# Optimization experiments

Hardware: AMD Instinct MI355X
Metric: run time of the kernel (lower is better)

The kernel has to match this reference:

```python
import jax, jax.numpy as jnp
import numpy as np

V, T, C, H, L = 32000, 1024, 768, 12, 6
HS = C // H
B = 4
EPS = 1e-5


def layernorm(x, g, b):
    mu = jnp.mean(x, axis=-1, keepdims=True)
    var = jnp.mean(jnp.square(x - mu), axis=-1, keepdims=True)
    return (x - mu) * jax.lax.rsqrt(var + EPS) * g + b


def setup_inputs() -> dict:
    key = jax.random.key(0)
    ks = iter(jax.random.split(key, 24))
    s = lambda *sh: jax.random.normal(next(ks), sh, dtype=jnp.float32) * 0.02
    inp = {
        "tokens": jax.random.randint(next(ks), (B, T), 0, V, dtype=jnp.int64),
        "tok_emb": s(V, C),
        "pos_emb": s(T, C),
        "ln1_g": jnp.ones((L, C), jnp.float32), "ln1_b": jnp.zeros((L, C), jnp.float32),
        "wq": s(L, C, C), "wk": s(L, C, C), "wv": s(L, C, C),
        "wo": s(L, C, C), "bo": jnp.zeros((L, C), jnp.float32),
        "ln2_g": jnp.ones((L, C), jnp.float32), "ln2_b": jnp.zeros((L, C), jnp.float32),
        "w1": s(L, C, 4 * C), "b1": jnp.zeros((L, 4 * C), jnp.float32),
        "w2": s(L, 4 * C, C), "b2": jnp.zeros((L, C), jnp.float32),
        "lnf_g": jnp.ones((C,), jnp.float32), "lnf_b": jnp.zeros((C,), jnp.float32),
        "lm_w": s(C, V), "lm_b": jnp.zeros((V,), jnp.float32),
    }
    return inp


def reference(tokens, tok_emb, pos_emb, ln1_g, ln1_b, wq, wk, wv, wo, bo,
              ln2_g, ln2_b, w1, b1, w2, b2, lnf_g, lnf_b, lm_w, lm_b):
    x = tok_emb[tokens] + pos_emb[:T]  # [B,T,C]
    causal = jnp.tril(jnp.ones((T, T), bool))
    scale = HS ** -0.5
    for l in range(L):
        h = layernorm(x, ln1_g[l], ln1_b[l])
        q = (h @ wq[l]).reshape(B, T, H, HS)
        k = (h @ wk[l]).reshape(B, T, H, HS)
        v = (h @ wv[l]).reshape(B, T, H, HS)
        att = jnp.einsum("bthd,bshd->bhts", q, k) * scale
        att = jnp.where(causal, att, -jnp.inf)
        wei = jax.nn.softmax(att, axis=-1)
        o = jnp.einsum("bhts,bshd->bthd", wei, v).reshape(B, T, C)
        x = o @ wo[l] + bo[l] + x
        h2 = layernorm(x, ln2_g[l], ln2_b[l])
        x = jax.nn.relu(h2 @ w1[l] + b1[l]) @ w2[l] + b2[l] + x
    x = layernorm(x, lnf_g, lnf_b)
    logits = x @ lm_w + lm_b  # [B,T,V]
    return logits
```

## Files before the change

### kernel.cpp

```cpp
#include <hip/hip_runtime.h>

static constexpr int kV = 32000, kT = 1024, kC = 768, kH = 12, kL = 6, kB = 4;
static constexpr int kF = 3072;
static constexpr int kM = kB * kT;
static constexpr float kNEG = -30000.f;

typedef __attribute__((ext_vector_type(8))) __bf16 bf16x8;
typedef __attribute__((ext_vector_type(4))) float  f32x4;

#define DEV __device__ __forceinline__

DEV void gload16(const void* g, void* l) {
  __builtin_amdgcn_global_load_lds((__attribute__((address_space(1))) void*)(g),
                                   (__attribute__((address_space(3))) void*)(l), 16, 0, 0);
}

__global__ __launch_bounds__(192) void embed_k(const int* __restrict__ tokens,
                                               const float* __restrict__ tok_emb,
                                               const float* __restrict__ pos_emb,
                                               float* __restrict__ x) {
  int row = blockIdx.x, tid = threadIdx.x;
  int tok = tokens[row];
  int t   = row & (kT - 1);
  const float4* te = (const float4*)(tok_emb + (size_t)tok * kC);
  const float4* pe = (const float4*)(pos_emb + (size_t)t * kC);
  float4 a = te[tid], p = pe[tid];
  float4 r; r.x = a.x + p.x; r.y = a.y + p.y; r.z = a.z + p.z; r.w = a.w + p.w;
  ((float4*)(x + (size_t)row * kC))[tid] = r;
}

__global__ __launch_bounds__(192) void ln_k(const float* __restrict__ x,
                                            const float* __restrict__ g,
                                            const float* __restrict__ b,
                                            __bf16* __restrict__ out) {
  int row = blockIdx.x, tid = threadIdx.x;
  float4 v = ((const float4*)(x + (size_t)row * kC))[tid];
  float s = v.x + v.y + v.z + v.w;
#pragma unroll
  for (int m = 1; m < 64; m <<= 1) s += __shfl_xor(s, m, 64);
  __shared__ float red1[3], red2[3];
  int wid = tid >> 6;
  if ((tid & 63) == 0) red1[wid] = s;
  __syncthreads();
  float mu = (red1[0] + red1[1] + red1[2]) * (1.f / kC);
  float d0 = v.x - mu, d1 = v.y - mu, d2 = v.z - mu, d3 = v.w - mu;
  float q = d0 * d0 + d1 * d1 + d2 * d2 + d3 * d3;
#pragma unroll
  for (int m = 1; m < 64; m <<= 1) q += __shfl_xor(q, m, 64);
  if ((tid & 63) == 0) red2[wid] = q;
  __syncthreads();
  float var = (red2[0] + red2[1] + red2[2]) * (1.f / kC);
  float rs = rsqrtf(var + 1e-5f);
  float4 gv = ((const float4*)g)[tid];
  float4 bv = ((const float4*)b)[tid];
  float o0 = d0 * rs * gv.x + bv.x;
  float o1 = d1 * rs * gv.y + bv.y;
  float o2 = d2 * rs * gv.z + bv.z;
  float o3 = d3 * rs * gv.w + bv.w;
  ushort4 pk;
  unsigned short* pp = (unsigned short*)&pk;
  __bf16 t0 = (__bf16)o0; pp[0] = *(unsigned short*)&t0;
  __bf16 t1 = (__bf16)o1; pp[1] = *(unsigned short*)&t1;
  __bf16 t2 = (__bf16)o2; pp[2] = *(unsigned short*)&t2;
  __bf16 t3 = (__bf16)o3; pp[3] = *(unsigned short*)&t3;
  ((ushort4*)(out + (size_t)row * kC))[tid] = pk;
}

__global__ __launch_bounds__(256) void convT_k(const float* __restrict__ in,
                                               __bf16* __restrict__ out,
                                               int R, int Cc, size_t in_ls, size_t out_ls) {
  __shared__ float tile[32][33];
  const float* inp  = in  + (size_t)blockIdx.z * in_ls;
  __bf16*      outp = out + (size_t)blockIdx.z * out_ls;
  int r0 = blockIdx.y * 32, c0 = blockIdx.x * 32;
  int tx = threadIdx.x & 31, ty = threadIdx.x >> 5;
#pragma unroll
  for (int i = 0; i < 32; i += 8)
    tile[ty + i][tx] = inp[(size_t)(r0 + ty + i) * Cc + c0 + tx];
  __syncthreads();
  int wx = threadIdx.x & 15, wy = threadIdx.x >> 4;
#pragma unroll
  for (int i = 0; i < 32; i += 16) {
    int oc = wy + i;
    __bf16 a = (__bf16)tile[wx * 2][oc];
    __bf16 c = (__bf16)tile[wx * 2 + 1][oc];
    ushort2 pk;
    unsigned short* pp = (unsigned short*)&pk;
    pp[0] = *(unsigned short*)&a;
    pp[1] = *(unsigned short*)&c;
    *(ushort2*)(&outp[(size_t)(c0 + oc) * R + r0 + wx * 2]) = pk;
  }
}

__global__ __launch_bounds__(256) void convT3_k(const float* __restrict__ wq,
                                                const float* __restrict__ wk,
                                                const float* __restrict__ wv,
                                                __bf16* __restrict__ qkvT) {
  __shared__ float tile[32][33];
  int z = blockIdx.z, layer = z / 3, which = z % 3;
  const float* inp = (which == 0 ? wq : which == 1 ? wk : wv) + (size_t)layer * kC * kC;
  __bf16* outp = qkvT + (size_t)layer * 3 * kC * kC + (size_t)which * kC * kC;
  int r0 = blockIdx.y * 32, c0 = blockIdx.x * 32;
  int tx = threadIdx.x & 31, ty = threadIdx.x >> 5;
#pragma unroll
  for (int i = 0; i < 32; i += 8)
    tile[ty + i][tx] = inp[(size_t)(r0 + ty + i) * kC + c0 + tx];
  __syncthreads();
  int wx = threadIdx.x & 15, wy = threadIdx.x >> 4;
#pragma unroll
  for (int i = 0; i < 32; i += 16) {
    int oc = wy + i;
    __bf16 a = (__bf16)tile[wx * 2][oc];
    __bf16 c = (__bf16)tile[wx * 2 + 1][oc];
    ushort2 pk;
    unsigned short* pp = (unsigned short*)&pk;
    pp[0] = *(unsigned short*)&a;
    pp[1] = *(unsigned short*)&c;
    *(ushort2*)(&outp[(size_t)(c0 + oc) * kC + r0 + wx * 2]) = pk;
  }
}

DEV void tile_decode(int gx, int gy, int& mt, int& nt) {
  int nwg  = gx * gy;
  int wgid = blockIdx.y * gx + blockIdx.x;
  int q8 = nwg >> 3;
  int xcd = wgid & 7, loc = wgid >> 3;
  int sid = xcd * q8 + loc;
  int band = gx << 3;
  int c = sid / band, rem = sid % band;
  nt = rem >> 3;
  mt = (c << 3) + (rem & 7);
}

__global__ __launch_bounds__(512, 1) void gemmHD_k(const __bf16* __restrict__ A,
                                                   const __bf16* __restrict__ Bt,
                                                   const float* __restrict__ bias,
                                                   float* __restrict__ Cout,
                                                   int M, int N, int K) {
  __shared__ char lds[131072];
  int tid = threadIdx.x, lane = tid & 63, wid = tid >> 6;
  int wm = wid >> 2, wn = wid & 3;
  int mt, ntile;
  tile_decode(gridDim.x, gridDim.y, mt, ntile);
  int m0 = mt * 256, n0 = ntile * 256;
  int fr = lane & 15, fg = lane >> 4;
  f32x4 acc[8][4] = {};
  const size_t ldab = (size_t)K * 2;
  int nt = K >> 6;

  auto STAGE = [&](char* base, int t) {
    int k0 = t << 6;
#pragma unroll
    for (int it = 0; it < 4; ++it) {
      int oo  = tid * 16 + it * 8192;
      int row = oo >> 7;
      int cb  = (oo & 127) ^ ((row & 7) << 4);
      gload16((const char*)A + (size_t)(m0 + row) * ldab + (size_t)k0 * 2 + cb,
              base + it * 8192 + wid * 1024);
    }
#pragma unroll
    for (int it = 0; it < 4; ++it) {
      int oo  = tid * 16 + it * 8192;
      int row = oo >> 7;
      int cb  = (oo & 127) ^ ((row & 7) << 4);
      gload16((const char*)Bt + (size_t)(n0 + row) * ldab + (size_t)k0 * 2 + cb,
              base + 32768 + it * 8192 + wid * 1024);
    }
  };

  STAGE(lds, 0);
  asm volatile("s_waitcnt vmcnt(0)" ::: "memory");
  __builtin_amdgcn_sched_barrier(0);
  __builtin_amdgcn_s_barrier();

  for (int t = 0; t < nt; ++t) {
    char* base = lds + (t & 1) * 65536;
    const char* Ab = base;
    const char* Bb = base + 32768;
    if (t + 1 < nt) STAGE(lds + ((t + 1) & 1) * 65536, t + 1);

    __builtin_amdgcn_s_setprio(1);
    bf16x8 bfr[4];
#pragma unroll
    for (int p = 0; p < 4; ++p) {
      const int ks = p >> 1, mh = p & 1;
      const int cc = ks * 64 + fg * 16;
      if (mh == 0) {
#pragma unroll
        for (int n = 0; n < 4; ++n) {
          int row = wn * 64 + n * 16 + fr;
          bfr[n] = *(const bf16x8*)(Bb + row * 128 + (cc ^ ((row & 7) << 4)));
        }
      }
      bf16x8 af[4];
#pragma unroll
      for (int i = 0; i < 4; ++i) {
        int row = wm * 128 + mh * 64 + i * 16 + fr;
        af[i] = *(const bf16x8*)(Ab + row * 128 + (cc ^ ((row & 7) << 4)));
      }
#pragma unroll
      for (int i = 0; i < 4; ++i)
#pragma unroll
        for (int n = 0; n < 4; ++n)
          acc[mh * 4 + i][n] = __builtin_amdgcn_mfma_f32_16x16x32_bf16(
              af[i], bfr[n], acc[mh * 4 + i][n], 0, 0, 0);
    }
    __builtin_amdgcn_s_setprio(0);

    __builtin_amdgcn_s_barrier();
    if (t + 1 < nt)
      asm volatile("s_waitcnt vmcnt(0)" ::: "memory");
    __builtin_amdgcn_sched_barrier(0);
    __builtin_amdgcn_s_barrier();
  }

#pragma unroll
  for (int mi = 0; mi < 8; ++mi) {
#pragma unroll
    for (int n = 0; n < 4; ++n) {
      int cg  = n0 + wn * 64 + n * 16 + fr;
      int rgb = m0 + wm * 128 + mi * 16 + fg * 4;
      float bv = bias[cg];
#pragma unroll
      for (int r = 0; r < 4; ++r)
        Cout[(size_t)(rgb + r) * N + cg] = acc[mi][n][r] + bv;
    }
  }
}

template <int EPI>
__global__ __launch_bounds__(256) void gemm128_k(const __bf16* __restrict__ A,
                                                 const __bf16* __restrict__ Bt,
                                                 const float* __restrict__ bias,
                                                 const float* res,
                                                 void* Cout,
                                                 int M, int N, int K) {
  __shared__ char lds[65536];
  int tid = threadIdx.x, lane = tid & 63, wid = tid >> 6;
  int wr = wid >> 1, wc = wid & 1;
  int mt, ntile;
  tile_decode(gridDim.x, gridDim.y, mt, ntile);
  int m0 = mt * 128, n0 = ntile * 128;
  int fr = lane & 15, fg = lane >> 4;
  f32x4 acc[4][4] = {};
  const size_t ldab = (size_t)K * 2;

  auto STAGE = [&](int buf, int t) {
    int k0 = t << 6;
    char* base = lds + buf * 32768;
#pragma unroll
    for (int it = 0; it < 4; ++it) {
      int oo  = tid * 16 + it * 4096;
      int row = oo >> 7;
      int cb  = (oo & 127) ^ ((row & 7) << 4);
      gload16((const char*)A  + (size_t)(m0 + row) * ldab + (size_t)k0 * 2 + cb,
              base + it * 4096 + wid * 1024);
      gload16((const char*)Bt + (size_t)(n0 + row) * ldab + (size_t)k0 * 2 + cb,
              base + 16384 + it * 4096 + wid * 1024);
    }
  };
  auto COMPUTE = [&](int buf) {
    char* base = lds + buf * 32768;
#pragma unroll
    for (int kk = 0; kk < 2; ++kk) {
      int cb = (kk * 64 + (fg << 4)) ^ ((lane & 7) << 4);
      bf16x8 af[4], bfr[4];
#pragma unroll
      for (int i = 0; i < 4; ++i) {
        af[i]  = *(const bf16x8*)(base         + (wr * 64 + i * 16 + fr) * 128 + cb);
        bfr[i] = *(const bf16x8*)(base + 16384 + (wc * 64 + i * 16 + fr) * 128 + cb);
      }
#pragma unroll
      for (int i = 0; i < 4; ++i)
#pragma unroll
        for (int j = 0; j < 4; ++j)
          acc[i][j] = __builtin_amdgcn_mfma_f32_16x16x32_bf16(af[i], bfr[j], acc[i][j], 0, 0, 0);
    }
  };

  int nt = K >> 6;
  STAGE(0, 0);
  STAGE(1, 1);
  asm volatile("s_waitcnt vmcnt(8)" ::: "memory");
  __builtin_amdgcn_sched_barrier(0);
  __builtin_amdgcn_s_barrier();
  int cur = 0;
  for (int t = 0; t < nt; ++t) {
    __builtin_amdgcn_s_setprio(1);
    COMPUTE(cur);
    __builtin_amdgcn_s_setprio(0);
    if (t + 1 < nt) {
      __builtin_amdgcn_s_barrier();
      if (t + 2 < nt) {
        STAGE(cur, t + 2);
        asm volatile("s_waitcnt vmcnt(8)" ::: "memory");
      } else {
        asm volatile("s_waitcnt vmcnt(0)" ::: "memory");
      }
      __builtin_amdgcn_sched_barrier(0);
      __builtin_amdgcn_s_barrier();
      cur ^= 1;
    }
  }

#pragma unroll
  for (int i = 0; i < 4; ++i) {
#pragma unroll
    for (int j = 0; j < 4; ++j) {
      int cg  = n0 + wc * 64 + j * 16 + fr;
      int rgb = m0 + wr * 64 + i * 16 + fg * 4;
      if constexpr (EPI == 4) {
        if (n0 < 1536) {
#pragma unroll
          for (int r = 0; r < 4; ++r)
            ((__bf16*)Cout)[(size_t)(rgb + r) * 1536 + cg] = (__bf16)acc[i][j][r];
        } else {
          int d = cg - 1536;
          ushort4 pk;
          unsigned short* pp = (unsigned short*)&pk;
#pragma unroll
          for (int r = 0; r < 4; ++r) {
            __bf16 bv = (__bf16)acc[i][j][r];
            pp[r] = *(unsigned short*)&bv;
          }
          __bf16* vT = (__bf16*)const_cast<float*>(res);
          *(ushort4*)(vT + (size_t)d * kM + rgb) = pk;
        }
      } else {
        float bv = bias[cg];
#pragma unroll
        for (int r = 0; r < 4; ++r) {
          float v = acc[i][j][r] + bv;
          ((__bf16*)Cout)[(size_t)(rgb + r) * N + cg] = (__bf16)fmaxf(v, 0.f);
        }
      }
    }
  }
}

__global__ __launch_bounds__(256) void gemm64_k(const __bf16* __restrict__ A,
                                                const __bf16* __restrict__ Bt,
                                                const float* __restrict__ bias,
                                                const float* res,
                                                float* __restrict__ Cout,
                                                int M, int N, int K) {
  __shared__ char lds[49152];
  int tid = threadIdx.x, lane = tid & 63, wid = tid >> 6;
  int wr = wid >> 1, wc = wid & 1;
  int mt, ntile;
  tile_decode(gridDim.x, gridDim.y, mt, ntile);
  int m0 = mt * 128, n0 = ntile * 64;
  int fr = lane & 15, fg = lane >> 4;
  f32x4 acc[4][2] = {};
  const size_t ldab = (size_t)K * 2;

  auto STAGE = [&](int buf, int t) {
    int k0 = t << 6;
    char* base = lds + buf * 24576;
#pragma unroll
    for (int it = 0; it < 4; ++it) {
      int oo  = tid * 16 + it * 4096;
      int row = oo >> 7;
      int cb  = (oo & 127) ^ ((row & 7) << 4);
      gload16((const char*)A + (size_t)(m0 + row) * ldab + (size_t)k0 * 2 + cb,
              base + it * 4096 + wid * 1024);
    }
#pragma unroll
    for (int it = 0; it < 2; ++it) {
      int oo  = tid * 16 + it * 4096;
      int row = oo >> 7;
      int cb  = (oo & 127) ^ ((row & 7) << 4);
      gload16((const char*)Bt + (size_t)(n0 + row) * ldab + (size_t)k0 * 2 + cb,
              base + 16384 + it * 4096 + wid * 1024);
    }
  };
  auto COMPUTE = [&](int buf) {
    char* base = lds + buf * 24576;
#pragma unroll
    for (int kk = 0; kk < 2; ++kk) {
      int cb = (kk * 64 + (fg << 4)) ^ ((lane & 7) << 4);
      bf16x8 af[4], bfr[2];
#pragma unroll
      for (int i = 0; i < 4; ++i)
        af[i] = *(const bf16x8*)(base + (wr * 64 + i * 16 + fr) * 128 + cb);
#pragma unroll
      for (int j = 0; j < 2; ++j)
        bfr[j] = *(const bf16x8*)(base + 16384 + (wc * 32 + j * 16 + fr) * 128 + cb);
#pragma unroll
      for (int i = 0; i < 4; ++i)
#pragma unroll
        for (int j = 0; j < 2; ++j)
          acc[i][j] = __builtin_amdgcn_mfma_f32_16x16x32_bf16(af[i], bfr[j], acc[i][j], 0, 0, 0);
    }
  };

  int nt = K >> 6;
  STAGE(0, 0);
  STAGE(1, 1);
  asm volatile("s_waitcnt vmcnt(6)" ::: "memory");
  __builtin_amdgcn_sched_barrier(0);
  __builtin_amdgcn_s_barrier();
  int cur = 0;
  for (int t = 0; t < nt; ++t) {
    __builtin_amdgcn_s_setprio(1);
    COMPUTE(cur);
    __builtin_amdgcn_s_setprio(0);
    if (t + 1 < nt) {
      __builtin_amdgcn_s_barrier();
      if (t + 2 < nt) {
        STAGE(cur, t + 2);
        asm volatile("s_waitcnt vmcnt(6)" ::: "memory");
      } else {
        asm volatile("s_waitcnt vmcnt(0)" ::: "memory");
      }
      __builtin_amdgcn_sched_barrier(0);
      __builtin_amdgcn_s_barrier();
      cur ^= 1;
    }
  }

#pragma unroll
  for (int i = 0; i < 4; ++i) {
#pragma unroll
    for (int j = 0; j < 2; ++j) {
      int cg  = n0 + wc * 32 + j * 16 + fr;
      int rgb = m0 + wr * 64 + i * 16 + fg * 4;
      float bv = bias[cg];
#pragma unroll
      for (int r = 0; r < 4; ++r) {
        float v = acc[i][j][r] + bv;
        size_t idx = (size_t)(rgb + r) * N + cg;
        Cout[idx] = v + res[idx];
      }
    }
  }
}

__global__ __launch_bounds__(256) void attn_k(const __bf16* __restrict__ qk,
                                              const __bf16* __restrict__ vT,
                                              __bf16* __restrict__ optr) {
  __shared__ char lds[40960];
  int tid = threadIdx.x, lane = tid & 63, wid = tid >> 6;
  int hh = blockIdx.y, bb = blockIdx.z;
  int band = (bb * 12 + hh) >> 4;
  int xx = blockIdx.x;
  int qt;
  if (band == 0)      qt = ((xx & 7) << 1) | (xx >> 3);
  else if (band == 1) qt = (xx < 8) ? (7 - xx) : (23 - xx);
  else                qt = 15 - xx;
  size_t rowbase = (size_t)bb * kT;
  int qr = qt * 64 + wid * 16;
  char* Psw = lds + 32768 + wid * 2048;

  bf16x8 qf[2];
  {
    const __bf16* p = qk + (rowbase + qr + (lane & 15)) * (2 * kC) + hh * 64 + ((lane >> 4) * 8);
    qf[0] = *(const bf16x8*)p;
    qf[1] = *(const bf16x8*)(p + 32);
  }
  f32x4 oacc[4] = {};
  float mrun[4] = {kNEG, kNEG, kNEG, kNEG};
  float lrun[4] = {0.f, 0.f, 0.f, 0.f};

  bf16x8 kr[2], vr[2];
  auto LOADT = [&](int st) {
    int s0 = st * 64;
#pragma unroll
    for (int it = 0; it < 2; ++it) {
      int oo  = tid * 16 + it * 4096;
      int row = oo >> 7;
      int cb  = (oo & 127) ^ ((row & 7) << 4);
      kr[it] = *(const bf16x8*)((const char*)qk +
                 ((rowbase + s0 + row) * (2 * kC) + kC + hh * 64) * 2 + cb);
      vr[it] = *(const bf16x8*)((const char*)vT +
                 ((size_t)(hh * 64 + row) * kM + rowbase + s0) * 2 + cb);
    }
  };
  auto WRITET = [&](int buf) {
    char* b = lds + buf * 16384;
#pragma unroll
    for (int it = 0; it < 2; ++it) {
      int oo = tid * 16 + it * 4096;
      *(bf16x8*)(b + oo)        = kr[it];
      *(bf16x8*)(b + 8192 + oo) = vr[it];
    }
  };

  LOADT(0);
  WRITET(0);
  if (qt >= 1) LOADT(1);

  for (int st = 0; st <= qt; ++st) {
    int cur = st & 1;
    char* kb = lds + cur * 16384;
    char* vb = kb + 8192;
    __syncthreads();
    if (st + 1 <= qt) {
      WRITET(cur ^ 1);
      if (st + 2 <= qt) LOADT(st + 2);
    }

    int s0 = st * 64;
    f32x4 sacc[4] = {};
#pragma unroll
    for (int kk = 0; kk < 2; ++kk) {
      int cb = (kk * 64 + ((lane >> 4) << 4)) ^ ((lane & 7) << 4);
#pragma unroll
      for (int j = 0; j < 4; ++j) {
        bf16x8 kf = *(const bf16x8*)(kb + (j * 16 + (lane & 15)) * 128 + cb);
        sacc[j] = __builtin_amdgcn_mfma_f32_16x16x32_bf16(qf[kk], kf, sacc[j], 0, 0, 0);
      }
    }

    float pv[4][4], vm[4] = {kNEG, kNEG, kNEG, kNEG};
#pragma unroll
    for (int j = 0; j < 4; ++j) {
      int scol = s0 + j * 16 + (lane & 15);
#pragma unroll
      for (int r = 0; r < 4; ++r) {
        int qrow = qr + (lane >> 4) * 4 + r;
        float sv = sacc[j][r] * 0.125f;
        if (scol > qrow) sv = kNEG;
        pv[j][r] = sv;
        vm[r] = fmaxf(vm[r], sv);
      }
    }
#pragma unroll
    for (int r = 0; r < 4; ++r) {
      float v = vm[r];
      v = fmaxf(v, __shfl_xor(v, 1, 64)); v = fmaxf(v, __shfl_xor(v, 2, 64));
      v = fmaxf(v, __shfl_xor(v, 4, 64)); v = fmaxf(v, __shfl_xor(v, 8, 64));
      float mnew = fmaxf(mrun[r], v);
      float sc = __expf(mrun[r] - mnew);
      mrun[r] = mnew;
      lrun[r] *= sc;
      oacc[0][r] *= sc; oacc[1][r] *= sc; oacc[2][r] *= sc; oacc[3][r] *= sc;
      float rsum = 0.f;
#pragma unroll
      for (int j = 0; j < 4; ++j) {
        float p = __expf(pv[j][r] - mnew);
        pv[j][r] = p;
        rsum += p;
      }
      rsum += __shfl_xor(rsum, 1, 64); rsum += __shfl_xor(rsum, 2, 64);
      rsum += __shfl_xor(rsum, 4, 64); rsum += __shfl_xor(rsum, 8, 64);
      lrun[r] += rsum;
    }

#pragma unroll
    for (int j = 0; j < 4; ++j)
#pragma unroll
      for (int r = 0; r < 4; ++r) {
        int rloc = (lane >> 4) * 4 + r;
        int cbyt = (2 * (j * 16 + (lane & 15))) ^ ((rloc & 7) << 4);
        *(__bf16*)(Psw + rloc * 128 + cbyt) = (__bf16)pv[j][r];
      }

#pragma unroll
    for (int kk = 0; kk < 2; ++kk) {
      int cb = (kk * 64 + ((lane >> 4) << 4)) ^ ((lane & 7) << 4);
      bf16x8 pf = *(const bf16x8*)(Psw + (lane & 15) * 128 + cb);
#pragma unroll
      for (int j = 0; j < 4; ++j) {
        bf16x8 vf = *(const bf16x8*)(vb + (j * 16 + (lane & 15)) * 128 + cb);
        oacc[j] = __builtin_amdgcn_mfma_f32_16x16x32_bf16(pf, vf, oacc[j], 0, 0, 0);
      }
    }
  }

#pragma unroll
  for (int r = 0; r < 4; ++r) {
    float inv = lrun[r] > 0.f ? 1.f / lrun[r] : 0.f;
#pragma unroll
    for (int j = 0; j < 4; ++j) {
      int cg = hh * 64 + j * 16 + (lane & 15);
      int rg = qr + (lane >> 4) * 4 + r;
      optr[(rowbase + rg) * kC + cg] = (__bf16)(oacc[j][r] * inv);
    }
  }
}

extern "C" void kernel_launch(void* const* d_in, const int* in_sizes, int n_in,
                              void* d_out, int out_size, void* d_ws, size_t ws_size,
                              hipStream_t stream) {
  (void)in_sizes; (void)n_in; (void)out_size; (void)ws_size;
  const int*   tokens  = (const int*)  d_in[0];
  const float* tok_emb = (const float*)d_in[1];
  const float* pos_emb = (const float*)d_in[2];
  const float* ln1_g   = (const float*)d_in[3];
  const float* ln1_b   = (const float*)d_in[4];
  const float* wq      = (const float*)d_in[5];
  const float* wk      = (const float*)d_in[6];
  const float* wv      = (const float*)d_in[7];
  const float* wo      = (const float*)d_in[8];
  const float* bo      = (const float*)d_in[9];
  const float* ln2_g   = (const float*)d_in[10];
  const float* ln2_b   = (const float*)d_in[11];
  const float* w1      = (const float*)d_in[12];
  const float* b1      = (const float*)d_in[13];
  const float* w2      = (const float*)d_in[14];
  const float* b2      = (const float*)d_in[15];
  const float* lnf_g   = (const float*)d_in[16];
  const float* lnf_b   = (const float*)d_in[17];
  const float* lm_w    = (const float*)d_in[18];
  const float* lm_b    = (const float*)d_in[19];
  float* out = (float*)d_out;

  char* ws = (char*)d_ws;
  size_t off = 0;
  auto alloc = [&](size_t bytes) -> char* {
    char* p = ws + off; off += (bytes + 255) & ~(size_t)255; return p;
  };
  float*  x    = (float*) alloc((size_t)kM * kC * 4);
  __bf16* h    = (__bf16*)alloc((size_t)kM * kC * 2);
  __bf16* qkvT = (__bf16*)alloc((size_t)kL * 3 * kC * kC * 2);
  __bf16* woT  = (__bf16*)alloc((size_t)kL * kC * kC * 2);
  __bf16* w1T  = (__bf16*)alloc((size_t)kL * kC * kF * 2);
  __bf16* w2T  = (__bf16*)alloc((size_t)kL * kC * kF * 2);
  __bf16* qkb  = (__bf16*)alloc((size_t)kM * 2 * kC * 2);
  __bf16* vTb  = (__bf16*)alloc((size_t)kC * kM * 2);
  __bf16* ob   = (__bf16*)alloc((size_t)kM * kC * 2);
  __bf16* ffb  = (__bf16*)alloc((size_t)kM * kF * 2);
  __bf16* lmwT = qkb;

  dim3 blk(256), blk512(512);
  convT3_k<<<dim3(kC/32, kC/32, 3*kL), blk, 0, stream>>>(wq, wk, wv, qkvT);
  convT_k<<<dim3(kC/32, kC/32, kL), blk, 0, stream>>>(wo, woT, kC, kC, (size_t)kC*kC, (size_t)kC*kC);
  convT_k<<<dim3(kF/32, kC/32, kL), blk, 0, stream>>>(w1, w1T, kC, kF, (size_t)kC*kF, (size_t)kC*kF);
  convT_k<<<dim3(kC/32, kF/32, kL), blk, 0, stream>>>(w2, w2T, kF, kC, (size_t)kC*kF, (size_t)kC*kF);

  embed_k<<<kM, 192, 0, stream>>>(tokens, tok_emb, pos_emb, x);

  for (int l = 0; l < kL; ++l) {
    ln_k<<<kM, 192, 0, stream>>>(x, ln1_g + l*kC, ln1_b + l*kC, h);
    gemm128_k<4><<<dim3(3*kC/128, kM/128), blk, 0, stream>>>(
        h, qkvT + (size_t)l*3*kC*kC, nullptr, (const float*)vTb, qkb, kM, 3*kC, kC);
    attn_k<<<dim3(kT/64, kH, kB), blk, 0, stream>>>(qkb, vTb, ob);
    gemm64_k<<<dim3(kC/64, kM/128), blk, 0, stream>>>(ob, woT + (size_t)l*kC*kC, bo + l*kC, x, x, kM, kC, kC);
    ln_k<<<kM, 192, 0, stream>>>(x, ln2_g + l*kC, ln2_b + l*kC, h);
    gemm128_k<1><<<dim3(kF/128, kM/128), blk, 0, stream>>>(h, w1T + (size_t)l*kC*kF, b1 + l*kF, nullptr, ffb, kM, kF, kC);
    gemm64_k<<<dim3(kC/64, kM/128), blk, 0, stream>>>(ffb, w2T + (size_t)l*kC*kF, b2 + l*kC, x, x, kM, kC, kF);
  }
  convT_k<<<dim3(kV/32, kC/32, 1), blk, 0, stream>>>(lm_w, lmwT, kC, kV, 0, 0);
  ln_k<<<kM, 192, 0, stream>>>(x, lnf_g, lnf_b, h);
  gemmHD_k<<<dim3(kV/256, kM/256), blk512, 0, stream>>>(h, lmwT, lm_b, out, kM, kV, kC);
}
```

Baseline: 1.229 ms.

## Restructure 256x256 GEMM main loop into quadrant-staged ping-pong pipeline

```diff
diff --git a/kernel.cpp b/kernel.cpp
--- a/kernel.cpp
+++ b/kernel.cpp
@@ -148,71 +148,105 @@
   const size_t ldab = (size_t)K * 2;
   int nt = K >> 6;
 
-  auto STAGE = [&](char* base, int t) {
+  auto STAGEH = [&](int buf, int gr, const __bf16* src, int srow0, int t) {
     int k0 = t << 6;
-#pragma unroll
-    for (int it = 0; it < 4; ++it) {
+    char* base = lds + buf * 65536 + gr * 16384;
+#pragma unroll
+    for (int it = 0; it < 2; ++it) {
       int oo  = tid * 16 + it * 8192;
       int row = oo >> 7;
       int cb  = (oo & 127) ^ ((row & 7) << 4);
-      gload16((const char*)A + (size_t)(m0 + row) * ldab + (size_t)k0 * 2 + cb,
+      gload16((const char*)src + (size_t)(srow0 + row) * ldab + (size_t)k0 * 2 + cb,
               base + it * 8192 + wid * 1024);
     }
-#pragma unroll
-    for (int it = 0; it < 4; ++it) {
-      int oo  = tid * 16 + it * 8192;
-      int row = oo >> 7;
-      int cb  = (oo & 127) ^ ((row & 7) << 4);
-      gload16((const char*)Bt + (size_t)(n0 + row) * ldab + (size_t)k0 * 2 + cb,
-              base + 32768 + it * 8192 + wid * 1024);
-    }
-  };
-
-  STAGE(lds, 0);
-  asm volatile("s_waitcnt vmcnt(0)" ::: "memory");
+  };
+
+  bf16x8 aA[4][2], bB[2][2];
+  auto LDA = [&](int buf, int mh) {
+    const char* Ab = lds + buf * 65536 + wm * 16384;
+#pragma unroll
+    for (int mi = 0; mi < 4; ++mi)
+#pragma unroll
+      for (int k = 0; k < 2; ++k) {
+        int lr = mh * 64 + mi * 16 + fr;
+        aA[mi][k] = *(const bf16x8*)(Ab + lr * 128 + ((k * 64 + fg * 16) ^ ((lr & 7) << 4)));
+      }
+  };
+  auto LDB = [&](int buf, int nh) {
+    const char* Bb = lds + buf * 65536 + 32768 + (wn >> 1) * 16384;
+    int blr = (wn & 1) * 64;
+#pragma unroll
+    for (int nj = 0; nj < 2; ++nj)
+#pragma unroll
+      for (int k = 0; k < 2; ++k) {
+        int lr = blr + nh * 32 + nj * 16 + fr;
+        bB[nj][k] = *(const bf16x8*)(Bb + lr * 128 + ((k * 64 + fg * 16) ^ ((lr & 7) << 4)));
+      }
+  };
+  auto MFMAQ = [&](int mh, int nh) {
+    __builtin_amdgcn_s_setprio(1);
+#pragma unroll
+    for (int mi = 0; mi < 4; ++mi)
+#pragma unroll
+      for (int nj = 0; nj < 2; ++nj)
+#pragma unroll
+        for (int k = 0; k < 2; ++k)
+          acc[mh * 4 + mi][nh * 2 + nj] = __builtin_amdgcn_mfma_f32_16x16x32_bf16(
+              aA[mi][k], bB[nj][k], acc[mh * 4 + mi][nh * 2 + nj], 0, 0, 0);
+    __builtin_amdgcn_s_setprio(0);
+  };
+
+#define BAR() do { __builtin_amdgcn_s_barrier(); __builtin_amdgcn_sched_barrier(0); } while (0)
+
+  STAGEH(0, 0, A,  m0,       0);
+  STAGEH(0, 1, A,  m0 + 128, 0);
+  STAGEH(0, 2, Bt, n0,       0);
+  STAGEH(0, 3, Bt, n0 + 128, 0);
+  if (nt > 1) {
+    STAGEH(1, 0, A,  m0,       1);
+    STAGEH(1, 1, A,  m0 + 128, 1);
+    asm volatile("s_waitcnt vmcnt(4)" ::: "memory");
+  } else {
+    asm volatile("s_waitcnt vmcnt(0)" ::: "memory");
+  }
   __builtin_amdgcn_sched_barrier(0);
   __builtin_amdgcn_s_barrier();
 
   for (int t = 0; t < nt; ++t) {
-    char* base = lds + (t & 1) * 65536;
-    const char* Ab = base;
-    const char* Bb = base + 32768;
-    if (t + 1 < nt) STAGE(lds + ((t + 1) & 1) * 65536, t + 1);
-
-    __builtin_amdgcn_s_setprio(1);
-    bf16x8 bfr[4];
-#pragma unroll
-    for (int p = 0; p < 4; ++p) {
-      const int ks = p >> 1, mh = p & 1;
-      const int cc = ks * 64 + fg * 16;
-      if (mh == 0) {
-#pragma unroll
-        for (int n = 0; n < 4; ++n) {
-          int row = wn * 64 + n * 16 + fr;
-          bfr[n] = *(const bf16x8*)(Bb + row * 128 + (cc ^ ((row & 7) << 4)));
-        }
-      }
-      bf16x8 af[4];
-#pragma unroll
-      for (int i = 0; i < 4; ++i) {
-        int row = wm * 128 + mh * 64 + i * 16 + fr;
-        af[i] = *(const bf16x8*)(Ab + row * 128 + (cc ^ ((row & 7) << 4)));
-      }
-#pragma unroll
-      for (int i = 0; i < 4; ++i)
-#pragma unroll
-        for (int n = 0; n < 4; ++n)
-          acc[mh * 4 + i][n] = __builtin_amdgcn_mfma_f32_16x16x32_bf16(
-              af[i], bfr[n], acc[mh * 4 + i][n], 0, 0, 0);
-    }
-    __builtin_amdgcn_s_setprio(0);
-
+    int buf = t & 1;
+    LDA(buf, 0); LDB(buf, 0);
+    if (t + 1 < nt) {
+      STAGEH(buf ^ 1, 2, Bt, n0,       t + 1);
+      STAGEH(buf ^ 1, 3, Bt, n0 + 128, t + 1);
+    }
+    BAR();
+    MFMAQ(0, 0);
+    BAR();
+    LDB(buf, 1);
+    BAR();
+    MFMAQ(0, 1);
+    BAR();
+    LDA(buf, 1);
+    BAR();
+    MFMAQ(1, 1);
+    BAR();
+    LDB(buf, 0);
+    if (t + 2 < nt) {
+      STAGEH(buf, 0, A, m0,       t + 2);
+      STAGEH(buf, 1, A, m0 + 128, t + 2);
+    }
+    BAR();
+    MFMAQ(1, 0);
     __builtin_amdgcn_s_barrier();
-    if (t + 1 < nt)
-      asm volatile("s_waitcnt vmcnt(0)" ::: "memory");
+    if (t + 1 < nt) {
+      if (t + 2 < nt) asm volatile("s_waitcnt vmcnt(4)" ::: "memory");
+      else            asm volatile("s_waitcnt vmcnt(0)" ::: "memory");
+      __builtin_amdgcn_sched_barrier(0);
+      __builtin_amdgcn_s_barrier();
+    }
     __builtin_amdgcn_sched_barrier(0);
-    __builtin_amdgcn_s_barrier();
-  }
+  }
+#undef BAR
 
 #pragma unroll
   for (int mi = 0; mi < 8; ++mi) {
```

After: 1.234 ms. Within noise of the previous version (+0.4%).
